# Kernel optimization log

Measured on AMD Instinct MI355X. Metric: run time of the kernel, lower is better.

Reference implementation:

```python
import jax, jax.numpy as jnp
import numpy as np

B, S, F, E, A = 8192, 200, 128, 64, 64
H1, H2, H3 = 128, 64, 32
EPS = 1e-5


def setup_inputs() -> dict:
    key = jax.random.key(0)
    ks = jax.random.split(key, 24)
    w = lambda k, shape: jax.random.normal(k, shape, dtype=jnp.float32) * 0.05
    inp = {
        'candidate_features': jax.random.normal(ks[0], (B, F), dtype=jnp.float32),
        'history_features': jax.random.normal(ks[1], (B, S, F), dtype=jnp.float32),
        'history_length': jax.random.randint(ks[2], (B,), 1, S + 1, dtype=jnp.int32),
        # item embedding linear
        'Wi': w(ks[3], (F, E)), 'bi': jnp.zeros((E,), jnp.float32),
        # additive attention
        'Wq': w(ks[4], (E, A)), 'Wk': w(ks[5], (E, A)), 'Wv': w(ks[6], (A,)),
        # MLP layer 1 (3E -> H1) + BN
        'W1': w(ks[7], (3 * E, H1)), 'b1': jnp.zeros((H1,), jnp.float32),
        'g1': jnp.ones((H1,), jnp.float32), 'be1': jnp.zeros((H1,), jnp.float32),
        'm1': w(ks[8], (H1,)), 'v1': jax.random.uniform(ks[9], (H1,), jnp.float32, 0.5, 1.5),
        # MLP layer 2 (H1 -> H2) + BN
        'W2': w(ks[10], (H1, H2)), 'b2': jnp.zeros((H2,), jnp.float32),
        'g2': jnp.ones((H2,), jnp.float32), 'be2': jnp.zeros((H2,), jnp.float32),
        'm2': w(ks[11], (H2,)), 'v2': jax.random.uniform(ks[12], (H2,), jnp.float32, 0.5, 1.5),
        # MLP layer 3 (H2 -> H3) + BN
        'W3': w(ks[13], (H2, H3)), 'b3': jnp.zeros((H3,), jnp.float32),
        'g3': jnp.ones((H3,), jnp.float32), 'be3': jnp.zeros((H3,), jnp.float32),
        'm3': w(ks[14], (H3,)), 'v3': jax.random.uniform(ks[15], (H3,), jnp.float32, 0.5, 1.5),
        # output layer
        'Wo': w(ks[16], (H3, 1)), 'bo': jnp.zeros((1,), jnp.float32),
    }
    return inp


def _bn(x, g, be, m, v):
    # BatchNorm1d in eval mode (running stats)
    return (x - m) * jax.lax.rsqrt(v + EPS) * g + be


def reference(candidate_features, history_features, history_length,
              Wi, bi, Wq, Wk, Wv,
              W1, b1, g1, be1, m1, v1,
              W2, b2, g2, be2, m2, v2,
              W3, b3, g3, be3, m3, v3,
              Wo, bo):
    # item embedding
    cand = candidate_features @ Wi + bi          # [B, E]
    hist = history_features @ Wi + bi            # [B, S, E]

    # additive (Bahdanau) attention
    qh = cand @ Wq                               # [B, A]
    kh = hist @ Wk                               # [B, S, A]
    hidden = jax.nn.relu(qh[:, None, :] + kh)    # [B, S, A]
    scores = hidden @ Wv                         # [B, S]

    seq = jnp.arange(hist.shape[1])
    mask = seq[None, :] < history_length[:, None]  # [B, S] bool
    scores = jnp.where(mask, scores, -1e9)
    attn = jax.nn.softmax(scores, axis=1)        # [B, S]
    interest = jnp.einsum('bs,bse->be', attn, hist)  # [B, E]

    # mean pooling over valid history
    lens = history_length[:, None].astype(hist.dtype)
    avg = jnp.sum(hist * mask[:, :, None], axis=1) / lens  # [B, E]

    x = jnp.concatenate([interest, cand, avg], axis=1)     # [B, 3E]
    x = jax.nn.relu(_bn(x @ W1 + b1, g1, be1, m1, v1))
    x = jax.nn.relu(_bn(x @ W2 + b2, g2, be2, m2, v2))
    x = jax.nn.relu(_bn(x @ W3 + b3, g3, be3, m3, v3))
    logits = x @ Wo + bo                                   # [B, 1]
    return jax.nn.sigmoid(logits)[:, 0]                    # [B]
```

## Files before the change

### kernel.cpp

```cpp
#include <hip/hip_runtime.h>
#include <math.h>

#define Bn 8192
#define Sn 200
#define Fn 128
#define En 64
#define An 64
#define H1n 128
#define H2n 64
#define H3n 32
#define EPSn 1e-5f

typedef __attribute__((ext_vector_type(8))) short bf16x8;
typedef __attribute__((ext_vector_type(4))) float f32x4;

__device__ __forceinline__ uint pack_bf2(float a, float b) {
    uint ua = __float_as_uint(a), ub = __float_as_uint(b);
    ua += 0x7fffu + ((ua >> 16) & 1u);
    ub += 0x7fffu + ((ub >> 16) & 1u);
    return (ua >> 16) | (ub & 0xffff0000u);
}
__device__ __forceinline__ ushort bf16_1(float a) {
    uint u = __float_as_uint(a);
    u += 0x7fffu + ((u >> 16) & 1u);
    return (ushort)(u >> 16);
}

__device__ __forceinline__ void pack_frag(const float* __restrict__ src,
                                          ushort* __restrict__ dst,
                                          int p, int N, int nk) {
    int j = p & 7, l = (p >> 3) & 63, t = p >> 9;
    int k = t % nk, ct = t / nk;
    int row = k * 32 + 8 * (l >> 4) + j;
    int col = ct * 16 + (l & 15);
    dst[p] = bf16_1(src[row * N + col]);
}

__global__ void k_prep(
    const float* __restrict__ Wi, const float* __restrict__ bi,
    const float* __restrict__ Wk, const float* __restrict__ Wq,
    const float* __restrict__ W1, const float* __restrict__ W2,
    const float* __restrict__ W3,
    const float* __restrict__ b1, const float* __restrict__ g1,
    const float* __restrict__ be1, const float* __restrict__ m1,
    const float* __restrict__ v1,
    const float* __restrict__ b2, const float* __restrict__ g2,
    const float* __restrict__ be2, const float* __restrict__ m2,
    const float* __restrict__ v2,
    const float* __restrict__ b3, const float* __restrict__ g3,
    const float* __restrict__ be3, const float* __restrict__ m3,
    const float* __restrict__ v3,
    ushort* __restrict__ wikp, ushort* __restrict__ wiqp, float* __restrict__ bq,
    ushort* __restrict__ wip, ushort* __restrict__ w1p,
    ushort* __restrict__ w2p, ushort* __restrict__ w3p,
    float* __restrict__ al1, float* __restrict__ bt1,
    float* __restrict__ al2, float* __restrict__ bt2,
    float* __restrict__ al3, float* __restrict__ bt3) {
    const int blk = blockIdx.x, tid = threadIdx.x;
    if (blk < 32) {
        int idx = blk * 256 + tid;
        int j = idx & 7, l = (idx >> 3) & 63, t = idx >> 9;
        int k = t & 3, ct = t >> 2;
        int row = k * 32 + 8 * (l >> 4) + j;
        int col = ct * 16 + (l & 15);
        float sk = 0.f, sq = 0.f;
        for (int e = 0; e < En; ++e) {
            float w = Wi[row * En + e];
            sk = fmaf(w, Wk[e * An + col], sk);
            sq = fmaf(w, Wq[e * An + col], sq);
        }
        wikp[idx] = bf16_1(sk);
        wiqp[idx] = bf16_1(sq);
        if (idx < An) {
            float s = 0.f;
            for (int e = 0; e < En; ++e)
                s = fmaf(bi[e], Wq[e * An + idx] + Wk[e * An + idx], s);
            bq[idx] = s;
        }
    } else if (blk < 64) {
        pack_frag(Wi, wip, (blk - 32) * 256 + tid, 64, 4);
    } else if (blk < 160) {
        pack_frag(W1, w1p, (blk - 64) * 256 + tid, 128, 6);
    } else if (blk < 192) {
        pack_frag(W2, w2p, (blk - 160) * 256 + tid, 64, 4);
    } else if (blk < 200) {
        pack_frag(W3, w3p, (blk - 192) * 256 + tid, 32, 2);
    } else {
        if (tid < H1n) {
            float a = g1[tid] * rsqrtf(v1[tid] + EPSn);
            al1[tid] = a; bt1[tid] = (b1[tid] - m1[tid]) * a + be1[tid];
        } else if (tid < H1n + H2n) {
            int i = tid - H1n;
            float a = g2[i] * rsqrtf(v2[i] + EPSn);
            al2[i] = a; bt2[i] = (b2[i] - m2[i]) * a + be2[i];
        } else if (tid < H1n + H2n + H3n) {
            int i = tid - H1n - H2n;
            float a = g3[i] * rsqrtf(v3[i] + EPSn);
            al3[i] = a; bt3[i] = (b3[i] - m3[i]) * a + be3[i];
        }
    }
}

__global__ __launch_bounds__(256, 4) void k_embed(
    const float* __restrict__ cand, const ushort* __restrict__ wip,
    const ushort* __restrict__ wiqp, const float* __restrict__ bi,
    const float* __restrict__ bq, ushort* __restrict__ ce, float* __restrict__ qhb) {
    const int tid = threadIdx.x, wv = tid >> 6, lane = tid & 63;
    const int rb = blockIdx.x * 64;
    __shared__ uint c_l[64 * 64];
    for (int i = tid; i < 2048; i += 256) {
        int row = i >> 5, f4 = i & 31;
        float4 v = ((const float4*)(cand + (size_t)(rb + row) * Fn))[f4];
        uint2 pw; pw.x = pack_bf2(v.x, v.y); pw.y = pack_bf2(v.z, v.w);
        int dw = (2 * f4) ^ ((row & 7) << 2);
        *(uint2*)&c_l[row * 64 + dw] = pw;
    }
    __syncthreads();
    const int r = wv * 16 + (lane & 15);
    bf16x8 afr[4];
    #pragma unroll
    for (int k = 0; k < 4; ++k)
        afr[k] = *(const bf16x8*)&c_l[r * 64 + ((k * 16 + 4 * (lane >> 4)) ^ ((r & 7) << 2))];
    #pragma unroll
    for (int ct = 0; ct < 4; ++ct) {
        f32x4 acc = {0.f, 0.f, 0.f, 0.f};
        #pragma unroll
        for (int k = 0; k < 4; ++k) {
            bf16x8 bfr = *(const bf16x8*)&wip[((ct * 4 + k) * 64 + lane) * 8];
            acc = __builtin_amdgcn_mfma_f32_16x16x32_bf16(afr[k], bfr, acc, 0, 0, 0);
        }
        int col = ct * 16 + (lane & 15);
        float bic = bi[col];
        #pragma unroll
        for (int i = 0; i < 4; ++i) {
            int rg = rb + wv * 16 + (lane >> 4) * 4 + i;
            ce[(size_t)rg * 64 + col] = bf16_1(acc[i] + bic);
        }
    }
    #pragma unroll
    for (int ct = 0; ct < 4; ++ct) {
        f32x4 acc = {0.f, 0.f, 0.f, 0.f};
        #pragma unroll
        for (int k = 0; k < 4; ++k) {
            bf16x8 bfr = *(const bf16x8*)&wiqp[((ct * 4 + k) * 64 + lane) * 8];
            acc = __builtin_amdgcn_mfma_f32_16x16x32_bf16(afr[k], bfr, acc, 0, 0, 0);
        }
        int col = ct * 16 + (lane & 15);
        float bqc = bq[col];
        #pragma unroll
        for (int i = 0; i < 4; ++i) {
            int rg = rb + wv * 16 + (lane >> 4) * 4 + i;
            qhb[(size_t)rg * 64 + col] = acc[i] + bqc;
        }
    }
}

__global__ __launch_bounds__(256, 4) void k_main(
    const float* __restrict__ hist, const int* __restrict__ hlen,
    const float* __restrict__ qhb, const float* __restrict__ Wv,
    const ushort* __restrict__ wikp, ushort* __restrict__ ifav) {
    const int b = blockIdx.x;
    const int tid = threadIdx.x, wv = tid >> 6, lane = tid & 63;
    __shared__ uint wik_l[4096];
    __shared__ alignas(16) uint h_u[64 * 64];
    __shared__ alignas(16) float w_sc[64];

    const int len = hlen[b];
    const float* hb = hist + (size_t)b * Sn * Fn;
    const int sl32 = tid >> 5;
    const int f4l = tid & 31;

    float4 pv[4];
    #pragma unroll
    for (int q = 0; q < 4; ++q) {
        int row = 32 + 8 * q + sl32;
        pv[q] = (row < len) ? ((const float4*)(hb + (size_t)row * Fn))[f4l]
                            : make_float4(0.f, 0.f, 0.f, 0.f);
    }
    {
        const uint4* wp = (const uint4*)wikp;
        for (int q = tid; q < 1024; q += 256) {
            uint4 v = wp[q];
            int l = q & 63;
            int dw = (q * 4) ^ (((l >> 3) & 3) << 2);
            *(uint4*)&wik_l[dw] = v;
        }
    }
    float qhb_l[4], wv_l[4];
    #pragma unroll
    for (int ct = 0; ct < 4; ++ct) {
        qhb_l[ct] = qhb[(size_t)b * 64 + ct * 16 + (lane & 15)];
        wv_l[ct] = Wv[ct * 16 + (lane & 15)];
    }

    float m = -3.0e38f, d = 0.f;
    float accx = 0.f, accy = 0.f, sumx = 0.f, sumy = 0.f;
    const int nch = (len + 63) >> 6;

    for (int c = 0; c < nch; ++c) {
        const int sc0 = c * 64;
        #pragma unroll
        for (int q = 0; q < 4; ++q) {
            int sl = 8 * q + sl32;
            int sg = sc0 + sl;
            float4 v = (sg < len) ? ((const float4*)(hb + (size_t)sg * Fn))[f4l]
                                  : make_float4(0.f, 0.f, 0.f, 0.f);
            uint2 pw;
            pw.x = pack_bf2(v.x, v.y);
            pw.y = pack_bf2(v.z, v.w);
            int dw = (2 * f4l) ^ ((sl & 7) << 2);
            *(uint2*)&h_u[sl * 64 + dw] = pw;
        }
        #pragma unroll
        for (int q = 0; q < 4; ++q) {
            int sl = 32 + 8 * q + sl32;
            uint2 pw;
            pw.x = pack_bf2(pv[q].x, pv[q].y);
            pw.y = pack_bf2(pv[q].z, pv[q].w);
            int dw = (2 * f4l) ^ ((sl & 7) << 2);
            *(uint2*)&h_u[sl * 64 + dw] = pw;
        }
        if (c + 1 < nch) {
            const int nb = sc0 + 64 + 32;
            #pragma unroll
            for (int q = 0; q < 4; ++q) {
                int row = nb + 8 * q + sl32;
                pv[q] = (row < len) ? ((const float4*)(hb + (size_t)row * Fn))[f4l]
                                    : make_float4(0.f, 0.f, 0.f, 0.f);
            }
        }
        __syncthreads();
        {
            const int r = wv * 16 + (lane & 15);
            bf16x8 afr[4];
            #pragma unroll
            for (int k = 0; k < 4; ++k)
                afr[k] = *(const bf16x8*)&h_u[r * 64 + ((k * 16 + 4 * (lane >> 4)) ^ ((r & 7) << 2))];
            float contrib[4] = {0.f, 0.f, 0.f, 0.f};
            #pragma unroll
            for (int ct = 0; ct < 4; ++ct) {
                f32x4 acc = {0.f, 0.f, 0.f, 0.f};
                #pragma unroll
                for (int k = 0; k < 4; ++k) {
                    bf16x8 bfr = *(const bf16x8*)&wik_l[(((ct * 4 + k) * 64 + lane) * 4) ^ (((lane >> 3) & 3) << 2)];
                    acc = __builtin_amdgcn_mfma_f32_16x16x32_bf16(afr[k], bfr, acc, 0, 0, 0);
                }
                float qv = qhb_l[ct], wvv = wv_l[ct];
                #pragma unroll
                for (int rr = 0; rr < 4; ++rr)
                    contrib[rr] += fmaxf(acc[rr] + qv, 0.f) * wvv;
            }
            #pragma unroll
            for (int o = 1; o < 16; o <<= 1) {
                #pragma unroll
                for (int rr = 0; rr < 4; ++rr)
                    contrib[rr] += __shfl_xor(contrib[rr], o, 64);
            }
            if ((lane & 15) == 0) {
                #pragma unroll
                for (int rr = 0; rr < 4; ++rr) {
                    int jr = wv * 16 + (lane >> 4) * 4 + rr;
                    w_sc[jr] = (sc0 + jr < len) ? contrib[rr] : -1e30f;
                }
            }
        }
        __syncthreads();
        {
            const f32x4* wsp = (const f32x4*)w_sc;
            float mloc = -3.0e38f;
            #pragma unroll
            for (int q = 0; q < 16; ++q) {
                f32x4 s = wsp[q];
                mloc = fmaxf(mloc, fmaxf(fmaxf(s[0], s[1]), fmaxf(s[2], s[3])));
            }
            float mn = fmaxf(m, mloc);
            float cc = __expf(m - mn);
            m = mn;
            d *= cc; accx *= cc; accy *= cc;
            #pragma unroll
            for (int j = 0; j < 16; ++j) {
                int sl = 4 * j + wv;
                float wgt = __expf(w_sc[sl] - mn);
                d += wgt;
                uint hv = h_u[sl * 64 + (lane ^ ((sl & 7) << 2))];
                float hx = __uint_as_float(hv << 16);
                float hy = __uint_as_float(hv & 0xffff0000u);
                accx = fmaf(wgt, hx, accx);
                accy = fmaf(wgt, hy, accy);
                sumx += hx; sumy += hy;
            }
        }
        __syncthreads();
    }

    float* mrg = (float*)wik_l;
    if (lane == 0) mrg[wv] = d;
    mrg[8 + wv * Fn + 2 * lane + 0] = accx;
    mrg[8 + wv * Fn + 2 * lane + 1] = accy;
    mrg[520 + wv * Fn + 2 * lane + 0] = sumx;
    mrg[520 + wv * Fn + 2 * lane + 1] = sumy;
    __syncthreads();
    if (tid < Fn) {
        float D = mrg[0] + mrg[1] + mrg[2] + mrg[3];
        float A = mrg[8 + tid] + mrg[8 + Fn + tid] + mrg[8 + 2 * Fn + tid] + mrg[8 + 3 * Fn + tid];
        float S = mrg[520 + tid] + mrg[520 + Fn + tid] + mrg[520 + 2 * Fn + tid] + mrg[520 + 3 * Fn + tid];
        ifav[(size_t)b * 256 + tid] = bf16_1(A / D);
        ifav[(size_t)b * 256 + 128 + tid] = bf16_1(S / (float)len);
    }
}

__global__ __launch_bounds__(256, 2) void k_mlp(
    const ushort* __restrict__ ifav, const ushort* __restrict__ ce,
    const float* __restrict__ bi, const ushort* __restrict__ wip,
    const ushort* __restrict__ w1p, const ushort* __restrict__ w2p,
    const ushort* __restrict__ w3p,
    const float* __restrict__ al1, const float* __restrict__ bt1,
    const float* __restrict__ al2, const float* __restrict__ bt2,
    const float* __restrict__ al3, const float* __restrict__ bt3,
    const float* __restrict__ Wo, const float* __restrict__ bo,
    float* __restrict__ out) {
    const int tid = threadIdx.x, wv = tid >> 6, lane = tid & 63;
    const int rb = blockIdx.x * 64;
    __shared__ uint x_l[64 * 96];
    __shared__ uint h1_l[64 * 64];
    __shared__ uint h2_l[64 * 32];
    __shared__ uint h3_l[64 * 16];
    ushort* x_s = (ushort*)x_l;
    ushort* h1_s = (ushort*)h1_l;
    ushort* h2_s = (ushort*)h2_l;
    ushort* h3_s = (ushort*)h3_l;

    const int rloc = wv * 16 + (lane & 15);

    #pragma unroll
    for (int half = 0; half < 2; ++half) {
        bf16x8 afr[4];
        #pragma unroll
        for (int k = 0; k < 4; ++k)
            afr[k] = *(const bf16x8*)&ifav[(size_t)(rb + rloc) * 256 + half * 128 + k * 32 + 8 * (lane >> 4)];
        #pragma unroll
        for (int ct = 0; ct < 4; ++ct) {
            f32x4 acc = {0.f, 0.f, 0.f, 0.f};
            #pragma unroll
            for (int k = 0; k < 4; ++k) {
                bf16x8 bfr = *(const bf16x8*)&wip[((ct * 4 + k) * 64 + lane) * 8];
                acc = __builtin_amdgcn_mfma_f32_16x16x32_bf16(afr[k], bfr, acc, 0, 0, 0);
            }
            int col = ct * 16 + (lane & 15);
            float bic = bi[col];
            int xcol = half * 128 + col;
            #pragma unroll
            for (int i = 0; i < 4; ++i) {
                int row = wv * 16 + (lane >> 4) * 4 + i;
                int dd = (xcol >> 1) ^ ((row & 7) << 2);
                x_s[(row * 96 + dd) * 2 + (xcol & 1)] = bf16_1(acc[i] + bic);
            }
        }
    }
    {
        int rl = wv * 16 + (lane >> 2);
        int colb = (lane & 3) * 16;
        #pragma unroll
        for (int u = 0; u < 2; ++u) {
            uint4 v = *(const uint4*)&ce[(size_t)(rb + rl) * 64 + colb + u * 8];
            int db = (32 + (lane & 3) * 8 + u * 4) ^ ((rl & 7) << 2);
            *(uint4*)&x_l[rl * 96 + db] = v;
        }
    }
    {
        bf16x8 xa[6];
        #pragma unroll
        for (int k = 0; k < 6; ++k)
            xa[k] = *(const bf16x8*)&x_l[rloc * 96 + ((k * 16 + 4 * (lane >> 4)) ^ ((rloc & 7) << 2))];
        #pragma unroll
        for (int ct = 0; ct < 8; ++ct) {
            f32x4 acc = {0.f, 0.f, 0.f, 0.f};
            #pragma unroll
            for (int k = 0; k < 6; ++k) {
                bf16x8 bfr = *(const bf16x8*)&w1p[((ct * 6 + k) * 64 + lane) * 8];
                acc = __builtin_amdgcn_mfma_f32_16x16x32_bf16(xa[k], bfr, acc, 0, 0, 0);
            }
            int col = ct * 16 + (lane & 15);
            float a = al1[col], bt = bt1[col];
            #pragma unroll
            for (int i = 0; i < 4; ++i) {
                int row = wv * 16 + (lane >> 4) * 4 + i;
                float hv = fmaxf(fmaf(acc[i], a, bt), 0.f);
                int dd = (col >> 1) ^ ((row & 7) << 2);
                h1_s[(row * 64 + dd) * 2 + (col & 1)] = bf16_1(hv);
            }
        }
    }
    {
        bf16x8 xa[4];
        #pragma unroll
        for (int k = 0; k < 4; ++k)
            xa[k] = *(const bf16x8*)&h1_l[rloc * 64 + ((k * 16 + 4 * (lane >> 4)) ^ ((rloc & 7) << 2))];
        #pragma unroll
        for (int ct = 0; ct < 4; ++ct) {
            f32x4 acc = {0.f, 0.f, 0.f, 0.f};
            #pragma unroll
            for (int k = 0; k < 4; ++k) {
                bf16x8 bfr = *(const bf16x8*)&w2p[((ct * 4 + k) * 64 + lane) * 8];
                acc = __builtin_amdgcn_mfma_f32_16x16x32_bf16(xa[k], bfr, acc, 0, 0, 0);
            }
            int col = ct * 16 + (lane & 15);
            float a = al2[col], bt = bt2[col];
            #pragma unroll
            for (int i = 0; i < 4; ++i) {
                int row = wv * 16 + (lane >> 4) * 4 + i;
                float hv = fmaxf(fmaf(acc[i], a, bt), 0.f);
                int dd = (col >> 1) ^ ((row & 7) << 2);
                h2_s[(row * 32 + dd) * 2 + (col & 1)] = bf16_1(hv);
            }
        }
    }
    {
        bf16x8 xa[2];
        #pragma unroll
        for (int k = 0; k < 2; ++k)
            xa[k] = *(const bf16x8*)&h2_l[rloc * 32 + ((k * 16 + 4 * (lane >> 4)) ^ ((rloc & 7) << 2))];
        #pragma unroll
        for (int ct = 0; ct < 2; ++ct) {
            f32x4 acc = {0.f, 0.f, 0.f, 0.f};
            #pragma unroll
            for (int k = 0; k < 2; ++k) {
                bf16x8 bfr = *(const bf16x8*)&w3p[((ct * 2 + k) * 64 + lane) * 8];
                acc = __builtin_amdgcn_mfma_f32_16x16x32_bf16(xa[k], bfr, acc, 0, 0, 0);
            }
            int col = ct * 16 + (lane & 15);
            float a = al3[col], bt = bt3[col];
            #pragma unroll
            for (int i = 0; i < 4; ++i) {
                int row = wv * 16 + (lane >> 4) * 4 + i;
                float hv = fmaxf(fmaf(acc[i], a, bt), 0.f);
                int dd = (col >> 1) ^ ((row & 3) << 2);
                h3_s[(row * 16 + dd) * 2 + (col & 1)] = bf16_1(hv);
            }
        }
    }
    if (lane < 16) {
        int row = wv * 16 + lane;
        float acc = bo[0];
        #pragma unroll
        for (int dd = 0; dd < 16; ++dd) {
            uint hv = h3_l[row * 16 + (dd ^ ((row & 3) << 2))];
            float h0 = __uint_as_float(hv << 16);
            float h1 = __uint_as_float(hv & 0xffff0000u);
            acc = fmaf(h0, Wo[2 * dd], fmaf(h1, Wo[2 * dd + 1], acc));
        }
        out[rb + row] = 1.f / (1.f + __expf(-acc));
    }
}

extern "C" void kernel_launch(void* const* d_in, const int* in_sizes, int n_in,
                              void* d_out, int out_size, void* d_ws, size_t ws_size,
                              hipStream_t stream) {
    const float* cand = (const float*)d_in[0];
    const float* hist = (const float*)d_in[1];
    const int*   hlen = (const int*)d_in[2];
    const float* Wi = (const float*)d_in[3];
    const float* bi = (const float*)d_in[4];
    const float* Wq = (const float*)d_in[5];
    const float* Wk = (const float*)d_in[6];
    const float* Wv = (const float*)d_in[7];
    const float* W1 = (const float*)d_in[8];
    const float* b1 = (const float*)d_in[9];
    const float* g1 = (const float*)d_in[10];
    const float* be1 = (const float*)d_in[11];
    const float* m1 = (const float*)d_in[12];
    const float* v1 = (const float*)d_in[13];
    const float* W2 = (const float*)d_in[14];
    const float* b2 = (const float*)d_in[15];
    const float* g2 = (const float*)d_in[16];
    const float* be2 = (const float*)d_in[17];
    const float* m2 = (const float*)d_in[18];
    const float* v2 = (const float*)d_in[19];
    const float* W3 = (const float*)d_in[20];
    const float* b3 = (const float*)d_in[21];
    const float* g3 = (const float*)d_in[22];
    const float* be3 = (const float*)d_in[23];
    const float* m3 = (const float*)d_in[24];
    const float* v3 = (const float*)d_in[25];
    const float* Wo = (const float*)d_in[26];
    const float* bo = (const float*)d_in[27];
    float* out = (float*)d_out;

    char* ws = (char*)d_ws;
    ushort* wikp = (ushort*)(ws + 0);
    ushort* wiqp = (ushort*)(ws + 16384);
    ushort* wip  = (ushort*)(ws + 32768);
    ushort* w1p  = (ushort*)(ws + 49152);
    ushort* w2p  = (ushort*)(ws + 98304);
    ushort* w3p  = (ushort*)(ws + 114688);
    float*  bq   = (float*)(ws + 118784);
    float*  al1  = (float*)(ws + 119040);
    float*  bt1  = (float*)(ws + 119552);
    float*  al2  = (float*)(ws + 120064);
    float*  bt2  = (float*)(ws + 120320);
    float*  al3  = (float*)(ws + 120576);
    float*  bt3  = (float*)(ws + 120704);
    float*  qhb  = (float*)(ws + 131072);
    ushort* ce   = (ushort*)(ws + 131072 + 2097152);
    ushort* ifav = (ushort*)(ws + 131072 + 3145728);

    k_prep<<<201, 256, 0, stream>>>(Wi, bi, Wk, Wq, W1, W2, W3,
                                    b1, g1, be1, m1, v1,
                                    b2, g2, be2, m2, v2,
                                    b3, g3, be3, m3, v3,
                                    wikp, wiqp, bq, wip, w1p, w2p, w3p,
                                    al1, bt1, al2, bt2, al3, bt3);
    k_embed<<<Bn / 64, 256, 0, stream>>>(cand, wip, wiqp, bi, bq, ce, qhb);
    k_main<<<Bn, 256, 0, stream>>>(hist, hlen, qhb, Wv, wikp, ifav);
    k_mlp<<<Bn / 64, 256, 0, stream>>>(ifav, ce, bi, wip, w1p, w2p, w3p,
                                       al1, bt1, al2, bt2, al3, bt3, Wo, bo, out);
}
```

Baseline: 158.6 us.

## Process four batch rows per block in attention kernel, reusing staged Wk weights

k_main now handles ROWS=4 batch rows per workgroup, so the packed Wi·Wk weights are staged into LDS once per block instead of once per row. It also prefetches the next row's second half-chunk while the current row's results are merged and written, and merges through dedicated LDS arrays. The cost is a quarter as many blocks and serial per-row work inside a block. Uneven history lengths can also unbalance load across workgroups.

```diff
diff --git a/kernel.cpp b/kernel.cpp
--- a/kernel.cpp
+++ b/kernel.cpp
@@ -10,9 +10,14 @@
 #define H2n 64
 #define H3n 32
 #define EPSn 1e-5f
+#define ROWS 4
 
 typedef __attribute__((ext_vector_type(8))) short bf16x8;
 typedef __attribute__((ext_vector_type(4))) float f32x4;
+
+#define BARRL() do { asm volatile("s_waitcnt lgkmcnt(0)" ::: "memory"); \
+                     __builtin_amdgcn_s_barrier(); \
+                     asm volatile("" ::: "memory"); } while (0)
 
 __device__ __forceinline__ uint pack_bf2(float a, float b) {
     uint ua = __float_as_uint(a), ub = __float_as_uint(b);
@@ -159,16 +164,20 @@
     const float* __restrict__ hist, const int* __restrict__ hlen,
     const float* __restrict__ qhb, const float* __restrict__ Wv,
     const ushort* __restrict__ wikp, ushort* __restrict__ ifav) {
-    const int b = blockIdx.x;
     const int tid = threadIdx.x, wv = tid >> 6, lane = tid & 63;
     __shared__ uint wik_l[4096];
     __shared__ alignas(16) uint h_u[64 * 64];
     __shared__ alignas(16) float w_sc[64];
-
-    const int len = hlen[b];
-    const float* hb = hist + (size_t)b * Sn * Fn;
+    __shared__ float s_d[4];
+    __shared__ float s_acc[4][Fn];
+    __shared__ float s_sum[4][Fn];
+
     const int sl32 = tid >> 5;
     const int f4l = tid & 31;
+
+    int b = blockIdx.x * ROWS;
+    const float* hb = hist + (size_t)b * Sn * Fn;
+    int len = hlen[b];
 
     float4 pv[4];
     #pragma unroll
@@ -186,126 +195,143 @@
             *(uint4*)&wik_l[dw] = v;
         }
     }
-    float qhb_l[4], wv_l[4];
-    #pragma unroll
-    for (int ct = 0; ct < 4; ++ct) {
-        qhb_l[ct] = qhb[(size_t)b * 64 + ct * 16 + (lane & 15)];
-        wv_l[ct] = Wv[ct * 16 + (lane & 15)];
-    }
-
-    float m = -3.0e38f, d = 0.f;
-    float accx = 0.f, accy = 0.f, sumx = 0.f, sumy = 0.f;
-    const int nch = (len + 63) >> 6;
-
-    for (int c = 0; c < nch; ++c) {
-        const int sc0 = c * 64;
-        #pragma unroll
-        for (int q = 0; q < 4; ++q) {
-            int sl = 8 * q + sl32;
-            int sg = sc0 + sl;
-            float4 v = (sg < len) ? ((const float4*)(hb + (size_t)sg * Fn))[f4l]
-                                  : make_float4(0.f, 0.f, 0.f, 0.f);
-            uint2 pw;
-            pw.x = pack_bf2(v.x, v.y);
-            pw.y = pack_bf2(v.z, v.w);
-            int dw = (2 * f4l) ^ ((sl & 7) << 2);
-            *(uint2*)&h_u[sl * 64 + dw] = pw;
-        }
-        #pragma unroll
-        for (int q = 0; q < 4; ++q) {
-            int sl = 32 + 8 * q + sl32;
-            uint2 pw;
-            pw.x = pack_bf2(pv[q].x, pv[q].y);
-            pw.y = pack_bf2(pv[q].z, pv[q].w);
-            int dw = (2 * f4l) ^ ((sl & 7) << 2);
-            *(uint2*)&h_u[sl * 64 + dw] = pw;
-        }
-        if (c + 1 < nch) {
-            const int nb = sc0 + 64 + 32;
+
+    for (int r = 0; r < ROWS; ++r, ++b) {
+        float qhb_l[4], wv_l[4];
+        #pragma unroll
+        for (int ct = 0; ct < 4; ++ct) {
+            qhb_l[ct] = qhb[(size_t)b * 64 + ct * 16 + (lane & 15)];
+            wv_l[ct] = Wv[ct * 16 + (lane & 15)];
+        }
+
+        float m = -3.0e38f, d = 0.f;
+        float accx = 0.f, accy = 0.f, sumx = 0.f, sumy = 0.f;
+        const int nch = (len + 63) >> 6;
+
+        for (int c = 0; c < nch; ++c) {
+            const int sc0 = c * 64;
             #pragma unroll
             for (int q = 0; q < 4; ++q) {
-                int row = nb + 8 * q + sl32;
-                pv[q] = (row < len) ? ((const float4*)(hb + (size_t)row * Fn))[f4l]
-                                    : make_float4(0.f, 0.f, 0.f, 0.f);
-            }
-        }
-        __syncthreads();
-        {
-            const int r = wv * 16 + (lane & 15);
-            bf16x8 afr[4];
-            #pragma unroll
-            for (int k = 0; k < 4; ++k)
-                afr[k] = *(const bf16x8*)&h_u[r * 64 + ((k * 16 + 4 * (lane >> 4)) ^ ((r & 7) << 2))];
-            float contrib[4] = {0.f, 0.f, 0.f, 0.f};
-            #pragma unroll
-            for (int ct = 0; ct < 4; ++ct) {
-                f32x4 acc = {0.f, 0.f, 0.f, 0.f};
+                int sl = 8 * q + sl32;
+                int sg = sc0 + sl;
+                float4 v = (sg < len) ? ((const float4*)(hb + (size_t)sg * Fn))[f4l]
+                                      : make_float4(0.f, 0.f, 0.f, 0.f);
+                uint2 pw;
+                pw.x = pack_bf2(v.x, v.y);
+                pw.y = pack_bf2(v.z, v.w);
+                int dw = (2 * f4l) ^ ((sl & 7) << 2);
+                *(uint2*)&h_u[sl * 64 + dw] = pw;
+            }
+            #pragma unroll
+            for (int q = 0; q < 4; ++q) {
+                int sl = 32 + 8 * q + sl32;
+                uint2 pw;
+                pw.x = pack_bf2(pv[q].x, pv[q].y);
+                pw.y = pack_bf2(pv[q].z, pv[q].w);
+                int dw = (2 * f4l) ^ ((sl & 7) << 2);
+                *(uint2*)&h_u[sl * 64 + dw] = pw;
+            }
+            if (c + 1 < nch) {
+                const int nb = sc0 + 64 + 32;
                 #pragma unroll
-                for (int k = 0; k < 4; ++k) {
-                    bf16x8 bfr = *(const bf16x8*)&wik_l[(((ct * 4 + k) * 64 + lane) * 4) ^ (((lane >> 3) & 3) << 2)];
-                    acc = __builtin_amdgcn_mfma_f32_16x16x32_bf16(afr[k], bfr, acc, 0, 0, 0);
+                for (int q = 0; q < 4; ++q) {
+                    int row = nb + 8 * q + sl32;
+                    pv[q] = (row < len) ? ((const float4*)(hb + (size_t)row * Fn))[f4l]
+                                        : make_float4(0.f, 0.f, 0.f, 0.f);
                 }
-                float qv = qhb_l[ct], wvv = wv_l[ct];
+            }
+            __syncthreads();
+            {
+                const int rl = wv * 16 + (lane & 15);
+                bf16x8 afr[4];
                 #pragma unroll
-                for (int rr = 0; rr < 4; ++rr)
-                    contrib[rr] += fmaxf(acc[rr] + qv, 0.f) * wvv;
-            }
-            #pragma unroll
-            for (int o = 1; o < 16; o <<= 1) {
+                for (int k = 0; k < 4; ++k)
+                    afr[k] = *(const bf16x8*)&h_u[rl * 64 + ((k * 16 + 4 * (lane >> 4)) ^ ((rl & 7) << 2))];
+                float contrib[4] = {0.f, 0.f, 0.f, 0.f};
                 #pragma unroll
-                for (int rr = 0; rr < 4; ++rr)
-                    contrib[rr] += __shfl_xor(contrib[rr], o, 64);
-            }
-            if ((lane & 15) == 0) {
+                for (int ct = 0; ct < 4; ++ct) {
+                    f32x4 acc = {0.f, 0.f, 0.f, 0.f};
+                    #pragma unroll
+                    for (int k = 0; k < 4; ++k) {
+                        bf16x8 bfr = *(const bf16x8*)&wik_l[(((ct * 4 + k) * 64 + lane) * 4) ^ (((lane >> 3) & 3) << 2)];
+                        acc = __builtin_amdgcn_mfma_f32_16x16x32_bf16(afr[k], bfr, acc, 0, 0, 0);
+                    }
+                    float qv = qhb_l[ct], wvv = wv_l[ct];
+                    #pragma unroll
+                    for (int rr = 0; rr < 4; ++rr)
+                        contrib[rr] += fmaxf(acc[rr] + qv, 0.f) * wvv;
+                }
                 #pragma unroll
-                for (int rr = 0; rr < 4; ++rr) {
-                    int jr = wv * 16 + (lane >> 4) * 4 + rr;
-                    w_sc[jr] = (sc0 + jr < len) ? contrib[rr] : -1e30f;
+                for (int o = 1; o < 16; o <<= 1) {
+                    #pragma unroll
+                    for (int rr = 0; rr < 4; ++rr)
+                        contrib[rr] += __shfl_xor(contrib[rr], o, 64);
                 }
-            }
-        }
-        __syncthreads();
-        {
-            const f32x4* wsp = (const f32x4*)w_sc;
-            float mloc = -3.0e38f;
-            #pragma unroll
-            for (int q = 0; q < 16; ++q) {
-                f32x4 s = wsp[q];
-                mloc = fmaxf(mloc, fmaxf(fmaxf(s[0], s[1]), fmaxf(s[2], s[3])));
-            }
-            float mn = fmaxf(m, mloc);
-            float cc = __expf(m - mn);
-            m = mn;
-            d *= cc; accx *= cc; accy *= cc;
-            #pragma unroll
-            for (int j = 0; j < 16; ++j) {
-                int sl = 4 * j + wv;
-                float wgt = __expf(w_sc[sl] - mn);
-                d += wgt;
-                uint hv = h_u[sl * 64 + (lane ^ ((sl & 7) << 2))];
-                float hx = __uint_as_float(hv << 16);
-                float hy = __uint_as_float(hv & 0xffff0000u);
-                accx = fmaf(wgt, hx, accx);
-                accy = fmaf(wgt, hy, accy);
-                sumx += hx; sumy += hy;
-            }
-        }
-        __syncthreads();
-    }
-
-    float* mrg = (float*)wik_l;
-    if (lane == 0) mrg[wv] = d;
-    mrg[8 + wv * Fn + 2 * lane + 0] = accx;
-    mrg[8 + wv * Fn + 2 * lane + 1] = accy;
-    mrg[520 + wv * Fn + 2 * lane + 0] = sumx;
-    mrg[520 + wv * Fn + 2 * lane + 1] = sumy;
-    __syncthreads();
-    if (tid < Fn) {
-        float D = mrg[0] + mrg[1] + mrg[2] + mrg[3];
-        float A = mrg[8 + tid] + mrg[8 + Fn + tid] + mrg[8 + 2 * Fn + tid] + mrg[8 + 3 * Fn + tid];
-        float S = mrg[520 + tid] + mrg[520 + Fn + tid] + mrg[520 + 2 * Fn + tid] + mrg[520 + 3 * Fn + tid];
-        ifav[(size_t)b * 256 + tid] = bf16_1(A / D);
-        ifav[(size_t)b * 256 + 128 + tid] = bf16_1(S / (float)len);
+                if ((lane & 15) == 0) {
+                    #pragma unroll
+                    for (int rr = 0; rr < 4; ++rr) {
+                        int jr = wv * 16 + (lane >> 4) * 4 + rr;
+                        w_sc[jr] = (sc0 + jr < len) ? contrib[rr] : -1e30f;
+                    }
+                }
+            }
+            __syncthreads();
+            {
+                const f32x4* wsp = (const f32x4*)w_sc;
+                float mloc = -3.0e38f;
+                #pragma unroll
+                for (int q = 0; q < 16; ++q) {
+                    f32x4 s = wsp[q];
+                    mloc = fmaxf(mloc, fmaxf(fmaxf(s[0], s[1]), fmaxf(s[2], s[3])));
+                }
+                float mn = fmaxf(m, mloc);
+                float cc = __expf(m - mn);
+                m = mn;
+                d *= cc; accx *= cc; accy *= cc;
+                #pragma unroll
+                for (int j = 0; j < 16; ++j) {
+                    int sl = 4 * j + wv;
+                    float wgt = __expf(w_sc[sl] - mn);
+                    d += wgt;
+                    uint hv = h_u[sl * 64 + (lane ^ ((sl & 7) << 2))];
+                    float hx = __uint_as_float(hv << 16);
+                    float hy = __uint_as_float(hv & 0xffff0000u);
+                    accx = fmaf(wgt, hx, accx);
+                    accy = fmaf(wgt, hy, accy);
+                    sumx += hx; sumy += hy;
+                }
+            }
+            __syncthreads();
+        }
+
+        int nlen = 0;
+        const float* nhb = hb;
+        if (r + 1 < ROWS) {
+            nhb = hist + (size_t)(b + 1) * Sn * Fn;
+            nlen = hlen[b + 1];
+            #pragma unroll
+            for (int q = 0; q < 4; ++q) {
+                int row = 32 + 8 * q + sl32;
+                pv[q] = (row < nlen) ? ((const float4*)(nhb + (size_t)row * Fn))[f4l]
+                                     : make_float4(0.f, 0.f, 0.f, 0.f);
+            }
+        }
+
+        if (lane == 0) s_d[wv] = d;
+        s_acc[wv][2 * lane + 0] = accx;
+        s_acc[wv][2 * lane + 1] = accy;
+        s_sum[wv][2 * lane + 0] = sumx;
+        s_sum[wv][2 * lane + 1] = sumy;
+        BARRL();
+        if (tid < Fn) {
+            float D = s_d[0] + s_d[1] + s_d[2] + s_d[3];
+            float A = s_acc[0][tid] + s_acc[1][tid] + s_acc[2][tid] + s_acc[3][tid];
+            float S = s_sum[0][tid] + s_sum[1][tid] + s_sum[2][tid] + s_sum[3][tid];
+            ifav[(size_t)b * 256 + tid] = bf16_1(A / D);
+            ifav[(size_t)b * 256 + 128 + tid] = bf16_1(S / (float)len);
+        }
+        len = nlen;
+        hb = nhb;
     }
 }
 
@@ -511,7 +537,7 @@
                                     wikp, wiqp, bq, wip, w1p, w2p, w3p,
                                     al1, bt1, al2, bt2, al3, bt3);
     k_embed<<<Bn / 64, 256, 0, stream>>>(cand, wip, wiqp, bi, bq, ce, qhb);
-    k_main<<<Bn, 256, 0, stream>>>(hist, hlen, qhb, Wv, wikp, ifav);
+    k_main<<<Bn / ROWS, 256, 0, stream>>>(hist, hlen, qhb, Wv, wikp, ifav);
     k_mlp<<<Bn / 64, 256, 0, stream>>>(ifav, ce, bi, wip, w1p, w2p, w3p,
                                        al1, bt1, al2, bt2, al3, bt3, Wo, bo, out);
 }
```

Measured after the change: 189.9 us. +19.7%, slower.
